# Kernel tuning notes

Hardware: AMD Instinct MI355X
Metric: run time of the kernel (lower is better)

Reference implementation:

```python
import jax, jax.numpy as jnp
import numpy as np

DIM = 512
NUM_HEADS = 8
DIM_HEAD = DIM // NUM_HEADS


def _xavier(key, shape):
    fan_in, fan_out = shape[0], shape[1]
    a = (6.0 / (fan_in + fan_out)) ** 0.5
    return jax.random.uniform(key, shape, jnp.float32, -a, a)


def setup_inputs() -> dict:
    key = jax.random.key(0)
    ks = jax.random.split(key, 8)
    B, N, M = 2, 2048, 2048
    x = jax.random.normal(ks[0], (B, N, DIM), jnp.float32)
    source = jax.random.normal(ks[1], (B, M, DIM), jnp.float32)
    source_mask = jax.random.randint(ks[2], (B, M), 0, 2) > 0
    Wq = _xavier(ks[3], (DIM, DIM)); bq = jnp.zeros((DIM,), jnp.float32)
    Wk = _xavier(ks[4], (DIM, DIM)); bk = jnp.zeros((DIM,), jnp.float32)
    Wv = _xavier(ks[5], (DIM, DIM)); bv = jnp.zeros((DIM,), jnp.float32)
    Wm = _xavier(ks[6], (DIM, DIM)); bm = jnp.zeros((DIM,), jnp.float32)
    return {"x": x, "source": source, "source_mask": source_mask,
            "Wq": Wq, "bq": bq, "Wk": Wk, "bk": bk,
            "Wv": Wv, "bv": bv, "Wm": Wm, "bm": bm}


def reference(x, source, source_mask, Wq, bq, Wk, bk, Wv, bv, Wm, bm):
    B, N, D = x.shape
    M = source.shape[-2]
    H, Dh = NUM_HEADS, DIM_HEAD
    # projections (torch Linear: x @ W^T + b)
    q = (x @ Wq.T + bq).reshape(B, N, H, Dh)
    k = (source @ Wk.T + bk).reshape(B, M, H, Dh)
    v = (source @ Wv.T + bv).reshape(B, M, H, Dh)
    scale = 1.0 / (Dh ** 0.5)
    # scores: [B, N, M, H]
    scores = jnp.einsum('bnhd,bmhd->bnmh', q, k) * scale
    scores = jnp.where(source_mask[:, None, :, None], scores, -jnp.inf)
    prob = jax.nn.softmax(scores, axis=-2)  # softmax over m
    agg = jnp.einsum('bnmh,bmhd->bnhd', prob, v).reshape(B, N, D)
    return agg @ Wm.T + bm
```

## Files before the change

### kernel.cpp

```cpp
#include <hip/hip_runtime.h>
#include <hip/hip_bf16.h>

#define DIMF 512
#define NHEAD 8
#define DHEAD 64
#define BATCH 2
#define SEQN 2048
#define SEQM 2048
#define FPS 40
#define QSCALE 0.18033688011112042f

typedef unsigned short u16;
typedef __attribute__((ext_vector_type(8))) short bf16x8;
typedef __attribute__((ext_vector_type(4))) float f32x4;

static __device__ __forceinline__ u16 f2bf(float f) {
    unsigned u = __float_as_uint(f);
    u += 0x7FFF + ((u >> 16) & 1);
    return (u16)(u >> 16);
}
static __device__ __forceinline__ u16 f2bf_fast(float f) {
    return (u16)((__float_as_uint(f) + 0x8000u) >> 16);
}

static __device__ __forceinline__
void load16(const u16* g, u16* l) {
    __builtin_amdgcn_global_load_lds(
        (const __attribute__((address_space(1))) void*)g,
        (__attribute__((address_space(3))) void*)l,
        16, 0, 0);
}

__global__ __launch_bounds__(256)
void cvt_w(const float* __restrict__ wq, const float* __restrict__ wk,
           const float* __restrict__ wv, const float* __restrict__ wm,
           const int* __restrict__ mask,
           u16* __restrict__ wqb, u16* __restrict__ wkb,
           u16* __restrict__ wvb, u16* __restrict__ wmb,
           u16* __restrict__ maskbf)
{
    int i = (blockIdx.x * 256 + threadIdx.x) * 4;
    if (blockIdx.y == 4) {
        if (i < BATCH * SEQM) {
            int4 m4 = *(const int4*)&mask[i];
            *(ushort4*)&maskbf[i] = make_ushort4(m4.x ? 0x3F80 : 0, m4.y ? 0x3F80 : 0,
                                                 m4.z ? 0x3F80 : 0, m4.w ? 0x3F80 : 0);
        }
        return;
    }
    const float* in = (blockIdx.y == 0) ? wq : (blockIdx.y == 1) ? wk
                    : (blockIdx.y == 2) ? wv : wm;
    u16* out = (blockIdx.y == 0) ? wqb : (blockIdx.y == 1) ? wkb
             : (blockIdx.y == 2) ? wvb : wmb;
    if (i >= DIMF * DIMF) return;
    float4 v = *(const float4*)&in[i];
    *(ushort4*)&out[i] = make_ushort4(f2bf(v.x), f2bf(v.y), f2bf(v.z), f2bf(v.w));
}

__device__ __forceinline__
void gemm_mfma(const float* __restrict__ Xf, const u16* __restrict__ Xb,
               const u16* __restrict__ W, const float* __restrict__ bias,
               const int* __restrict__ msk, void* __restrict__ Out, int mode)
{
    __shared__ __align__(16) u16 SH[7680];
    u16* As = SH;
    u16* Bs = SH + 64 * FPS;

    const int tid  = threadIdx.x;
    const int wave = tid >> 6;
    const int lane = tid & 63;
    const int l15  = lane & 15;
    const int quad = lane >> 4;
    const int wm = wave & 1, wn = wave >> 1;
    const int r0 = blockIdx.x * 64, c0 = blockIdx.y * 128;

    f32x4 acc[2][4] = {};

    const int br = tid >> 2, boct = tid & 3;
    const int ar = tid >> 3, aseg = tid & 7;

    for (int k0 = 0; k0 < DIMF; k0 += 32) {
        bf16x8 bv0 = *(const bf16x8*)&W[(size_t)(c0 + br) * DIMF + k0 + boct * 8];
        bf16x8 bv1 = *(const bf16x8*)&W[(size_t)(c0 + br + 64) * DIMF + k0 + boct * 8];
        float4 a0, a1; bf16x8 av;
        if (Xf) {
            a0 = *(const float4*)&Xf[(size_t)(r0 + ar) * DIMF + k0 + aseg * 4];
            a1 = *(const float4*)&Xf[(size_t)(r0 + ar + 32) * DIMF + k0 + aseg * 4];
        } else {
            av = *(const bf16x8*)&Xb[(size_t)(r0 + br) * DIMF + k0 + boct * 8];
        }
        __syncthreads();
        if (Xf) {
            *(ushort4*)&As[ar * FPS + aseg * 4] =
                make_ushort4(f2bf(a0.x), f2bf(a0.y), f2bf(a0.z), f2bf(a0.w));
            *(ushort4*)&As[(ar + 32) * FPS + aseg * 4] =
                make_ushort4(f2bf(a1.x), f2bf(a1.y), f2bf(a1.z), f2bf(a1.w));
        } else {
            *(bf16x8*)&As[br * FPS + boct * 8] = av;
        }
        *(bf16x8*)&Bs[br * FPS + boct * 8] = bv0;
        *(bf16x8*)&Bs[(br + 64) * FPS + boct * 8] = bv1;
        __syncthreads();

        bf16x8 af[2], bf[4];
        #pragma unroll
        for (int mi = 0; mi < 2; ++mi)
            af[mi] = *(const bf16x8*)&As[(wm * 32 + mi * 16 + l15) * FPS + quad * 8];
        #pragma unroll
        for (int ni = 0; ni < 4; ++ni)
            bf[ni] = *(const bf16x8*)&Bs[(wn * 64 + ni * 16 + l15) * FPS + quad * 8];
        #pragma unroll
        for (int mi = 0; mi < 2; ++mi)
            #pragma unroll
            for (int ni = 0; ni < 4; ++ni)
                acc[mi][ni] = __builtin_amdgcn_mfma_f32_16x16x32_bf16(
                    af[mi], bf[ni], acc[mi][ni], 0, 0, 0);
    }

    float bb[4];
    #pragma unroll
    for (int ni = 0; ni < 4; ++ni)
        bb[ni] = bias[c0 + wn * 64 + ni * 16 + l15];

    if (mode == 2) {
        u16* T = SH;
        const int b = r0 >> 11;
        const int n_base = r0 & (SEQN - 1);
        #pragma unroll
        for (int hh = 0; hh < 2; ++hh) {
            __syncthreads();
            if (wn == hh) {
                #pragma unroll
                for (int mi = 0; mi < 2; ++mi) {
                    const int rl = wm * 32 + mi * 16 + quad * 4;
                    int4 m4 = *(const int4*)&msk[b * SEQM + n_base + rl];
                    float mm[4];
                    mm[0] = m4.x ? 1.f : 0.f; mm[1] = m4.y ? 1.f : 0.f;
                    mm[2] = m4.z ? 1.f : 0.f; mm[3] = m4.w ? 1.f : 0.f;
                    #pragma unroll
                    for (int ni = 0; ni < 4; ++ni)
                        #pragma unroll
                        for (int r = 0; r < 4; ++r)
                            T[(rl + r) * 72 + ni * 16 + l15] =
                                f2bf((acc[mi][ni][r] + bb[ni]) * mm[r]);
                }
            }
            __syncthreads();
            const int d = tid >> 2, ms = (tid & 3) << 4;
            u16 tmp[16];
            #pragma unroll
            for (int j = 0; j < 16; ++j) tmp[j] = T[(ms + j) * 72 + d];
            const int hgl = (c0 >> 6) + hh;
            u16* dst = (u16*)Out + ((size_t)(b * NHEAD + hgl) * DHEAD + d) * SEQM
                       + n_base + ms;
            *(bf16x8*)&dst[0] = *(bf16x8*)&tmp[0];
            *(bf16x8*)&dst[8] = *(bf16x8*)&tmp[8];
        }
        return;
    }

    #pragma unroll
    for (int mi = 0; mi < 2; ++mi) {
        const int Rbase = r0 + wm * 32 + mi * 16 + quad * 4;
        const int b = Rbase >> 11;
        const int nb = Rbase & (SEQN - 1);
        #pragma unroll
        for (int ni = 0; ni < 4; ++ni) {
            const int C = c0 + wn * 64 + ni * 16 + l15;
            const int h = C >> 6, d = C & 63;
            if (mode == 0) {
                u16* ow = (u16*)Out;
                #pragma unroll
                for (int r = 0; r < 4; ++r)
                    ow[(((size_t)(b * NHEAD + h) * SEQN) + nb + r) * DHEAD + d] =
                        f2bf((acc[mi][ni][r] + bb[ni]) * QSCALE);
            } else if (mode == 1) {
                u16* ow = (u16*)Out;
                #pragma unroll
                for (int r = 0; r < 4; ++r)
                    ow[(((size_t)(b * NHEAD + h) * SEQN) + nb + r) * DHEAD + d] =
                        f2bf(acc[mi][ni][r] + bb[ni]);
            } else {
                float* ow = (float*)Out;
                #pragma unroll
                for (int r = 0; r < 4; ++r)
                    ow[(size_t)(Rbase + r) * DIMF + C] = acc[mi][ni][r] + bb[ni];
            }
        }
    }
}

__global__ __launch_bounds__(256, 4)
void qkv_proj(const float* __restrict__ x, const float* __restrict__ src,
              const u16* __restrict__ wqb, const float* __restrict__ bq,
              const u16* __restrict__ wkb, const float* __restrict__ bk,
              const u16* __restrict__ wvb, const float* __restrict__ bv,
              const int* __restrict__ mask,
              u16* __restrict__ qw, u16* __restrict__ kw, u16* __restrict__ vtw)
{
    const int z = blockIdx.z;
    const float* X = (z == 0) ? x : src;
    const u16* W = (z == 0) ? wqb : (z == 1) ? wkb : wvb;
    const float* B = (z == 0) ? bq : (z == 1) ? bk : bv;
    void* O = (z == 0) ? (void*)qw : (z == 1) ? (void*)kw : (void*)vtw;
    gemm_mfma(X, nullptr, W, B, mask, O, z);
}

__global__ __launch_bounds__(256, 4)
void out_proj(const u16* __restrict__ aggb, const u16* __restrict__ wmb,
              const float* __restrict__ bm, float* __restrict__ out)
{
    gemm_mfma(nullptr, aggb, wmb, bm, nullptr, (void*)out, 3);
}

__global__ __launch_bounds__(256, 2)
void flash_attn_mfma(const u16* __restrict__ q, const u16* __restrict__ k,
                     const u16* __restrict__ vt, const u16* __restrict__ maskbf,
                     u16* __restrict__ agg)
{
    __shared__ __align__(16) u16 SH[13312];
    u16* Ks  = SH;
    u16* Vts = SH + 4096;
    u16* Ps  = SH + 8192;
    float* Osum = (float*)SH;
    float* Lsum = (float*)(SH + 8192);

    const int tid  = threadIdx.x;
    const int wave = tid >> 6;
    const int lane = tid & 63;
    const int l15  = lane & 15;
    const int quad = lane >> 4;
    const int qg = wave >> 1, mh = wave & 1;
    const int h = blockIdx.y, b = blockIdx.z;
    const int n0 = blockIdx.x * 64;
    const size_t hoff = (size_t)(b * NHEAD + h) * (size_t)SEQM * DHEAD;
    const u16* kb = k  + hoff;
    const u16* vb = vt + hoff;
    const u16* mb = maskbf + b * SEQM;

    const int dr   = lane >> 3;
    const int doct = (lane & 7) ^ (dr & 7);
    const int g0 = wave, g1 = 4 + wave;
    const u16* kq0 = kb + (size_t)(g0 * 8 + dr) * DHEAD + doct * 8;
    const u16* kq1 = kb + (size_t)(g1 * 8 + dr) * DHEAD + doct * 8;
    const u16* vq0 = vb + (size_t)(g0 * 8 + dr) * SEQM + doct * 8;
    const u16* vq1 = vb + (size_t)(g1 * 8 + dr) * SEQM + doct * 8;
    u16* kl0 = Ks  + g0 * 512;  u16* kl1 = Ks  + g1 * 512;
    u16* vl0 = Vts + g0 * 512;  u16* vl1 = Vts + g1 * 512;

    bf16x8 qf[2][2];
    #pragma unroll
    for (int qh = 0; qh < 2; ++qh) {
        const u16* qp = q + hoff + (size_t)(n0 + qg * 32 + qh * 16 + l15) * DHEAD
                        + quad * 8;
        qf[qh][0] = *(const bf16x8*)qp;
        qf[qh][1] = *(const bf16x8*)(qp + 32);
    }

    f32x4 O[2][4] = {};
    f32x4 lacc[2] = {};
    u16* Pw = Ps + wave * (32 * FPS);
    const int xoct = l15 & 7;

    for (int m0 = 0; m0 < SEQM; m0 += 64) {
        __syncthreads();
        load16(kq0 + (size_t)m0 * DHEAD, kl0);
        load16(kq1 + (size_t)m0 * DHEAD, kl1);
        load16(vq0 + m0, vl0);
        load16(vq1 + m0, vl1);
        __syncthreads();

        f32x4 st[2][2] = {};
        #pragma unroll
        for (int sub = 0; sub < 2; ++sub) {
            const int mrow = 32 * mh + 16 * sub + l15;
            #pragma unroll
            for (int c = 0; c < 2; ++c) {
                const int oct = (4 * c + quad) ^ xoct;
                bf16x8 af = *(const bf16x8*)&Ks[mrow * 64 + oct * 8];
                #pragma unroll
                for (int qh = 0; qh < 2; ++qh)
                    st[qh][sub] = __builtin_amdgcn_mfma_f32_16x16x32_bf16(
                        af, qf[qh][c], st[qh][sub], 0, 0, 0);
            }
        }

        #pragma unroll
        for (int qh = 0; qh < 2; ++qh)
            #pragma unroll
            for (int sub = 0; sub < 2; ++sub) {
                ushort4 w4 = make_ushort4(
                    f2bf_fast(__builtin_amdgcn_exp2f(st[qh][sub][0])),
                    f2bf_fast(__builtin_amdgcn_exp2f(st[qh][sub][1])),
                    f2bf_fast(__builtin_amdgcn_exp2f(st[qh][sub][2])),
                    f2bf_fast(__builtin_amdgcn_exp2f(st[qh][sub][3])));
                *(ushort4*)&Pw[(qh * 16 + l15) * FPS + 16 * sub + 4 * quad] = w4;
            }

        bf16x8 vf[4];
        #pragma unroll
        for (int sd = 0; sd < 4; ++sd) {
            const int oct = (4 * mh + quad) ^ xoct;
            vf[sd] = *(const bf16x8*)&Vts[(16 * sd + l15) * 64 + oct * 8];
        }
        bf16x8 mf = *(const bf16x8*)&mb[m0 + 32 * mh + quad * 8];

        #pragma unroll
        for (int qh = 0; qh < 2; ++qh) {
            bf16x8 pf = *(const bf16x8*)&Pw[(qh * 16 + l15) * FPS + quad * 8];
            lacc[qh] = __builtin_amdgcn_mfma_f32_16x16x32_bf16(pf, mf, lacc[qh], 0, 0, 0);
            #pragma unroll
            for (int sd = 0; sd < 4; ++sd)
                O[qh][sd] = __builtin_amdgcn_mfma_f32_16x16x32_bf16(
                    pf, vf[sd], O[qh][sd], 0, 0, 0);
        }
    }

    __syncthreads();
    if (mh == 1) {
        #pragma unroll
        for (int qh = 0; qh < 2; ++qh) {
            #pragma unroll
            for (int sd = 0; sd < 4; ++sd)
                #pragma unroll
                for (int r = 0; r < 4; ++r)
                    Osum[qg * 2048 + (qh * 16 + quad * 4 + r) * 64 + 16 * sd + l15]
                        = O[qh][sd][r];
            if (l15 == 0) {
                #pragma unroll
                for (int r = 0; r < 4; ++r)
                    Lsum[qg * 32 + qh * 16 + quad * 4 + r] = lacc[qh][r];
            }
        }
    }
    __syncthreads();
    if (mh == 0) {
        #pragma unroll
        for (int qh = 0; qh < 2; ++qh)
            #pragma unroll
            for (int r = 0; r < 4; ++r) {
                const float inv = 1.f /
                    (lacc[qh][r] + Lsum[qg * 32 + qh * 16 + quad * 4 + r]);
                const int n = n0 + qg * 32 + qh * 16 + quad * 4 + r;
                u16* ag = agg + ((size_t)b * SEQN + n) * DIMF + h * DHEAD + l15;
                #pragma unroll
                for (int sd = 0; sd < 4; ++sd)
                    ag[16 * sd] = f2bf((O[qh][sd][r] +
                        Osum[qg * 2048 + (qh * 16 + quad * 4 + r) * 64 + 16 * sd + l15])
                        * inv);
            }
    }
}

extern "C" void kernel_launch(void* const* d_in, const int* in_sizes, int n_in,
                              void* d_out, int out_size, void* d_ws, size_t ws_size,
                              hipStream_t stream)
{
    (void)in_sizes; (void)n_in; (void)out_size; (void)ws_size;
    const float* x      = (const float*)d_in[0];
    const float* source = (const float*)d_in[1];
    const int*   mask   = (const int*)  d_in[2];
    const float* Wq = (const float*)d_in[3]; const float* bq = (const float*)d_in[4];
    const float* Wk = (const float*)d_in[5]; const float* bk = (const float*)d_in[6];
    const float* Wv = (const float*)d_in[7]; const float* bv = (const float*)d_in[8];
    const float* Wm = (const float*)d_in[9]; const float* bm = (const float*)d_in[10];
    float* out = (float*)d_out;

    const size_t SZ = (size_t)BATCH * SEQN * DIMF;
    const size_t WZ = (size_t)DIMF * DIMF;
    u16* qw   = (u16*)d_ws;
    u16* kw   = qw  + SZ;
    u16* vtw  = kw  + SZ;
    u16* aggb = vtw + SZ;
    u16* wqb  = aggb + SZ;
    u16* wkb  = wqb + WZ;
    u16* wvb  = wkb + WZ;
    u16* wmb  = wvb + WZ;
    u16* maskbf = wmb + WZ;

    dim3 gcvt((WZ / 4 + 255) / 256, 5);
    cvt_w<<<gcvt, 256, 0, stream>>>(Wq, Wk, Wv, Wm, mask,
                                    wqb, wkb, wvb, wmb, maskbf);

    dim3 gproj(4096 / 64, 512 / 128, 3);
    qkv_proj<<<gproj, 256, 0, stream>>>(x, source, wqb, bq, wkb, bk, wvb, bv,
                                        mask, qw, kw, vtw);

    dim3 gattn(SEQN / 64, NHEAD, BATCH);
    flash_attn_mfma<<<gattn, 256, 0, stream>>>(qw, kw, vtw, maskbf, aggb);

    dim3 gout(4096 / 64, 512 / 128);
    out_proj<<<gout, 256, 0, stream>>>(aggb, wmb, bm, out);
}
```

Measured before the change: 154.3 us.

## Double-buffer K/V tiles in attention and remap blocks per XCD

The flash attention loop now double-buffers the K and V^T tiles in shared memory. The next tile and its mask fragment are loaded while the current one is computed, which cuts the loop to one barrier per iteration instead of two. The grid is also flattened to 1D and remapped so all query tiles of a given (batch, head) pair land on the same XCD, improving L2 reuse of K/V. Shared memory per block grows to about 42KB, which may reduce occupancy headroom.

```diff
diff --git a/kernel.cpp b/kernel.cpp
--- a/kernel.cpp
+++ b/kernel.cpp
@@ -218,12 +218,11 @@
                      const u16* __restrict__ vt, const u16* __restrict__ maskbf,
                      u16* __restrict__ agg)
 {
-    __shared__ __align__(16) u16 SH[13312];
-    u16* Ks  = SH;
-    u16* Vts = SH + 4096;
-    u16* Ps  = SH + 8192;
-    float* Osum = (float*)SH;
-    float* Lsum = (float*)(SH + 8192);
+    __shared__ __align__(16) u16 KsD[2][4096];
+    __shared__ __align__(16) u16 VtsD[2][4096];
+    __shared__ u16 Ps[4 * 32 * FPS];
+    float* Osum = (float*)&KsD[0][0];
+    float* Lsum = (float*)&VtsD[0][0];
 
     const int tid  = threadIdx.x;
     const int wave = tid >> 6;
@@ -231,8 +230,13 @@
     const int l15  = lane & 15;
     const int quad = lane >> 4;
     const int qg = wave >> 1, mh = wave & 1;
-    const int h = blockIdx.y, b = blockIdx.z;
-    const int n0 = blockIdx.x * 64;
+
+    const int bid  = blockIdx.x;
+    const int xcd  = bid & 7, slot = bid >> 3;
+    const int pair = (xcd << 1) | (slot & 1);
+    const int b = pair >> 3, h = pair & 7;
+    const int n0 = (slot >> 1) * 64;
+
     const size_t hoff = (size_t)(b * NHEAD + h) * (size_t)SEQM * DHEAD;
     const u16* kb = k  + hoff;
     const u16* vb = vt + hoff;
@@ -245,8 +249,6 @@
     const u16* kq1 = kb + (size_t)(g1 * 8 + dr) * DHEAD + doct * 8;
     const u16* vq0 = vb + (size_t)(g0 * 8 + dr) * SEQM + doct * 8;
     const u16* vq1 = vb + (size_t)(g1 * 8 + dr) * SEQM + doct * 8;
-    u16* kl0 = Ks  + g0 * 512;  u16* kl1 = Ks  + g1 * 512;
-    u16* vl0 = Vts + g0 * 512;  u16* vl1 = Vts + g1 * 512;
 
     bf16x8 qf[2][2];
     #pragma unroll
@@ -257,18 +259,32 @@
         qf[qh][1] = *(const bf16x8*)(qp + 32);
     }
 
+    load16(kq0, &KsD[0][g0 * 512]);
+    load16(kq1, &KsD[0][g1 * 512]);
+    load16(vq0, &VtsD[0][g0 * 512]);
+    load16(vq1, &VtsD[0][g1 * 512]);
+    bf16x8 mf_nxt = *(const bf16x8*)&mb[32 * mh + quad * 8];
+
     f32x4 O[2][4] = {};
     f32x4 lacc[2] = {};
     u16* Pw = Ps + wave * (32 * FPS);
     const int xoct = l15 & 7;
 
-    for (int m0 = 0; m0 < SEQM; m0 += 64) {
+    for (int mt = 0; mt < SEQM / 64; ++mt) {
+        const int cur = mt & 1;
         __syncthreads();
-        load16(kq0 + (size_t)m0 * DHEAD, kl0);
-        load16(kq1 + (size_t)m0 * DHEAD, kl1);
-        load16(vq0 + m0, vl0);
-        load16(vq1 + m0, vl1);
-        __syncthreads();
+        bf16x8 mf = mf_nxt;
+        if (mt + 1 < SEQM / 64) {
+            const int m1 = (mt + 1) * 64;
+            const int nb = cur ^ 1;
+            load16(kq0 + (size_t)m1 * DHEAD, &KsD[nb][g0 * 512]);
+            load16(kq1 + (size_t)m1 * DHEAD, &KsD[nb][g1 * 512]);
+            load16(vq0 + m1, &VtsD[nb][g0 * 512]);
+            load16(vq1 + m1, &VtsD[nb][g1 * 512]);
+            mf_nxt = *(const bf16x8*)&mb[m1 + 32 * mh + quad * 8];
+        }
+        const u16* Ks  = KsD[cur];
+        const u16* Vts = VtsD[cur];
 
         f32x4 st[2][2] = {};
         #pragma unroll
@@ -303,7 +319,6 @@
             const int oct = (4 * mh + quad) ^ xoct;
             vf[sd] = *(const bf16x8*)&Vts[(16 * sd + l15) * 64 + oct * 8];
         }
-        bf16x8 mf = *(const bf16x8*)&mb[m0 + 32 * mh + quad * 8];
 
         #pragma unroll
         for (int qh = 0; qh < 2; ++qh) {
@@ -386,8 +401,7 @@
     qkv_proj<<<gproj, 256, 0, stream>>>(x, source, wqb, bq, wkb, bk, wvb, bv,
                                         mask, qw, kw, vtw);
 
-    dim3 gattn(SEQN / 64, NHEAD, BATCH);
-    flash_attn_mfma<<<gattn, 256, 0, stream>>>(qw, kw, vtw, maskbf, aggb);
+    flash_attn_mfma<<<512, 256, 0, stream>>>(qw, kw, vtw, maskbf, aggb);
 
     dim3 gout(4096 / 64, 512 / 128);
     out_proj<<<gout, 256, 0, stream>>>(aggb, wmb, bm, out);
```

Measured after the change: 147.8 us. 1.04x faster.
